# Optimization experiments

Measured on AMD Instinct MI355X. Metric: run time of the kernel, lower is better.

## Reference

```python
import jax, jax.numpy as jnp
import numpy as np

V, E, U, B, T = 128, 256, 1024, 32, 256


def setup_inputs() -> dict:
    key = jax.random.key(0)
    ks = iter(jax.random.split(key, 64))
    def p(shape, scale=0.05):
        return jax.random.normal(next(ks), shape, jnp.float32) * scale
    inp = {
        "x": jax.random.randint(next(ks), (B, T), 0, V),
        "emb": p((V, E), 1.0),
        "fc_W": p((2 * U, V)),
        "fc_b": jnp.zeros((V,), jnp.float32),
    }
    for l in range(3):
        din = E if l == 0 else 2 * U
        for d in ("fw", "bw"):
            inp[f"Wg_{d}{l}"] = p((din + U, 2 * U))   # fused r,u gate kernel
            inp[f"bg_{d}{l}"] = jnp.ones((2 * U,), jnp.float32)  # TF GRUCell ones bias init
            inp[f"Wc_{d}{l}"] = p((din + U, U))       # candidate kernel
            inp[f"bc_{d}{l}"] = jnp.zeros((U,), jnp.float32)
            inp[f"h_{d}{l}"] = jnp.zeros((B, U), jnp.float32)
    return inp


def _gru_scan(x_seq, h0, Wg, bg, Wc, bc, reverse):
    # x_seq: [T, B, din]; TF contrib GRUCell math.
    def step(h, xt):
        ru = jax.nn.sigmoid(jnp.concatenate([xt, h], -1) @ Wg + bg)
        r, u = jnp.split(ru, 2, axis=-1)
        c = jnp.tanh(jnp.concatenate([xt, r * h], -1) @ Wc + bc)
        h_new = u * h + (1.0 - u) * c
        return h_new, h_new
    hT, ys = jax.lax.scan(step, h0, x_seq, reverse=reverse)
    return hT, ys  # ys in original time order even when reverse=True


def reference(x, emb, fc_W, fc_b,
              Wg_fw0, bg_fw0, Wc_fw0, bc_fw0, h_fw0,
              Wg_bw0, bg_bw0, Wc_bw0, bc_bw0, h_bw0,
              Wg_fw1, bg_fw1, Wc_fw1, bc_fw1, h_fw1,
              Wg_bw1, bg_bw1, Wc_bw1, bc_bw1, h_bw1,
              Wg_fw2, bg_fw2, Wc_fw2, bc_fw2, h_fw2,
              Wg_bw2, bg_bw2, Wc_bw2, bc_bw2, h_bw2):
    fw = [(Wg_fw0, bg_fw0, Wc_fw0, bc_fw0, h_fw0),
          (Wg_fw1, bg_fw1, Wc_fw1, bc_fw1, h_fw1),
          (Wg_fw2, bg_fw2, Wc_fw2, bc_fw2, h_fw2)]
    bw = [(Wg_bw0, bg_bw0, Wc_bw0, bc_bw0, h_bw0),
          (Wg_bw1, bg_bw1, Wc_bw1, bc_bw1, h_bw1),
          (Wg_bw2, bg_bw2, Wc_bw2, bc_bw2, h_bw2)]
    seq = emb[x].transpose(1, 0, 2)  # [T, B, E]
    states_fw, states_bw = [], []
    for l in range(3):
        Wg, bg, Wc, bc, h0 = fw[l]
        hf, yf = _gru_scan(seq, h0, Wg, bg, Wc, bc, reverse=False)
        Wg, bg, Wc, bc, h0 = bw[l]
        hb, yb = _gru_scan(seq, h0, Wg, bg, Wc, bc, reverse=True)
        seq = jnp.concatenate([yf, yb], axis=-1)  # [T, B, 2U]
        states_fw.append(hf)
        states_bw.append(hb)
    out = seq.transpose(1, 0, 2).reshape(-1, 2 * U)  # [B*T, 2U], batch-major like dynamic_rnn
    logits = out @ fc_W + fc_b
    return (logits, jnp.stack(states_fw), jnp.stack(states_bw))
```

## Files before the change

kernel.cpp:

```cpp
#include <hip/hip_runtime.h>

typedef _Float16 f16;
typedef _Float16 f16x4 __attribute__((ext_vector_type(4)));
typedef _Float16 f16x8 __attribute__((ext_vector_type(8)));
typedef float f32x4 __attribute__((ext_vector_type(4)));

#define NB 32
#define NT 256
#define NE 256
#define NU 1024
#define NV 128

#define MEMF() asm volatile("" ::: "memory")

__device__ __forceinline__ unsigned long long cload64(const f16* p) {
    return __hip_atomic_load((const unsigned long long*)p, __ATOMIC_RELAXED,
                             __HIP_MEMORY_SCOPE_AGENT);
}
__device__ __forceinline__ float cloadf(const float* p) {
    return __hip_atomic_load(p, __ATOMIC_RELAXED, __HIP_MEMORY_SCOPE_AGENT);
}
__device__ __forceinline__ void cstoref(float* p, float v) {
    __hip_atomic_store(p, v, __ATOMIC_RELAXED, __HIP_MEMORY_SCOPE_AGENT);
}
__device__ __forceinline__ void cstore16(f16* p, f16 v) {
    __hip_atomic_store((unsigned short*)p, __builtin_bit_cast(unsigned short, v),
                       __ATOMIC_RELAXED, __HIP_MEMORY_SCOPE_AGENT);
}

__device__ __forceinline__ void barsync() {
    MEMF();
    __builtin_amdgcn_s_barrier();
    MEMF();
}

__device__ __forceinline__ void gwait(const unsigned* flagd, unsigned target) {
    if (threadIdx.x < 64) {
        int it = 0;
        for (;;) {
            unsigned v = __hip_atomic_load(&flagd[(threadIdx.x & 31) * 16],
                                           __ATOMIC_RELAXED, __HIP_MEMORY_SCOPE_AGENT);
            if (__all(v >= target)) break;
            if (++it > (1 << 16)) break;
        }
    }
}

__device__ __forceinline__ void gbar(unsigned* flagd, int cg, unsigned target) {
    asm volatile("s_waitcnt vmcnt(0)" ::: "memory");
    barsync();
    if (threadIdx.x == 0)
        __hip_atomic_store(&flagd[cg * 16], target, __ATOMIC_RELAXED,
                           __HIP_MEMORY_SCOPE_AGENT);
    gwait(flagd, target);
    barsync();
}

__device__ __forceinline__ void stage16(const f16* __restrict__ src,
                                        f16* __restrict__ stg, int tid) {
    unsigned long long a[16];
    #pragma unroll
    for (int i = 0; i < 16; ++i)
        a[i] = cload64(src + i * NU + tid * 4);
    MEMF();
    #pragma unroll
    for (int i = 0; i < 16; ++i)
        *(f16x4*)(&stg[i * 1032 + tid * 4]) = __builtin_bit_cast(f16x4, a[i]);
}

__global__ void embed_kernel(const int* __restrict__ x, const float* __restrict__ emb,
                             f16* __restrict__ seq0) {
    int row = blockIdx.x;
    int t = row >> 5, b = row & 31;
    int e = threadIdx.x;
    int idx = x[b * NT + t];
    seq0[row * NE + e] = (f16)emb[idx * NE + e];
}

__global__ void wconv(const float* __restrict__ Wg, const float* __restrict__ Wc,
                      f16* __restrict__ WgT, f16* __restrict__ WcT, int K2) {
    __shared__ float tile[32][33];
    int mat = blockIdx.z & 1;
    const float* in = mat ? Wc : Wg;
    f16* outp = mat ? WcT : WgT;
    int N = mat ? 1024 : 2048;
    int by = blockIdx.y;
    if (by * 32 >= N) return;
    int k0 = blockIdx.x * 32, n0 = by * 32;
    int tx = threadIdx.x & 31, ty = threadIdx.x >> 5;
    #pragma unroll
    for (int i = 0; i < 4; ++i) {
        int r = ty * 4 + i;
        tile[r][tx] = in[(size_t)(k0 + r) * N + n0 + tx];
    }
    __syncthreads();
    #pragma unroll
    for (int i = 0; i < 4; ++i) {
        int rn = ty * 4 + i;
        outp[(size_t)(n0 + rn) * K2 + k0 + tx] = (f16)tile[tx][rn];
    }
}

__launch_bounds__(256)
__global__ void gemm_projT(const f16* __restrict__ A, int lda, int K,
                           const f16* __restrict__ WgT, const f16* __restrict__ WcT, int K2,
                           const float* __restrict__ bg, const float* __restrict__ bc,
                           f16* __restrict__ proj) {
    __shared__ f16 As[128][40];
    __shared__ f16 Bs[128][40];
    int cb = blockIdx.y;
    const f16* Bsrc; int outcol; const float* bias;
    if (cb < 16) { Bsrc = WgT + (size_t)cb * 128 * K2; outcol = cb * 128; bias = bg + cb * 128; }
    else { Bsrc = WcT + (size_t)(cb - 16) * 128 * K2; outcol = 2048 + (cb - 16) * 128; bias = bc + (cb - 16) * 128; }
    int m0 = blockIdx.x * 128;
    int tid = threadIdx.x;
    int w = tid >> 6, l = tid & 63;
    int wm = w & 1, wn = w >> 1;
    f32x4 acc[4][4] = {};
    for (int k0 = 0; k0 < K; k0 += 32) {
        __syncthreads();
        #pragma unroll
        for (int p = 0; p < 2; ++p) {
            int e = (p * 256 + tid) * 8;
            int r = e >> 5, kq = e & 31;
            f16x8 v = *(const f16x8*)(A + (size_t)(m0 + r) * lda + k0 + kq);
            *(f16x8*)(&As[r][kq]) = v;
        }
        #pragma unroll
        for (int p = 0; p < 2; ++p) {
            int e = (p * 256 + tid) * 8;
            int r = e >> 5, kq = e & 31;
            f16x8 v = *(const f16x8*)(Bsrc + (size_t)r * K2 + k0 + kq);
            *(f16x8*)(&Bs[r][kq]) = v;
        }
        __syncthreads();
        int kq = (l >> 4) * 8;
        f16x8 a[4], b[4];
        #pragma unroll
        for (int i = 0; i < 4; ++i) a[i] = *(const f16x8*)(&As[wm * 64 + i * 16 + (l & 15)][kq]);
        #pragma unroll
        for (int j = 0; j < 4; ++j) b[j] = *(const f16x8*)(&Bs[wn * 64 + j * 16 + (l & 15)][kq]);
        #pragma unroll
        for (int i = 0; i < 4; ++i)
            #pragma unroll
            for (int j = 0; j < 4; ++j)
                acc[i][j] = __builtin_amdgcn_mfma_f32_16x16x32_f16(a[i], b[j], acc[i][j], 0, 0, 0);
    }
    int lr = (l >> 4) * 4, lc = l & 15;
    #pragma unroll
    for (int i = 0; i < 4; ++i) {
        #pragma unroll
        for (int j = 0; j < 4; ++j) {
            int gcol = wn * 64 + j * 16 + lc;
            float bia = bias[gcol];
            #pragma unroll
            for (int q = 0; q < 4; ++q) {
                int grow = m0 + wm * 64 + i * 16 + lr + q;
                proj[(size_t)grow * 3072 + outcol + gcol] = (f16)(acc[i][j][q] + bia);
            }
        }
    }
}

__launch_bounds__(256)
__global__ void gemm_proj(const f16* __restrict__ A, int lda, int K,
                          const float* __restrict__ Wg, const float* __restrict__ Wc,
                          const float* __restrict__ bg, const float* __restrict__ bc,
                          f16* __restrict__ proj) {
    __shared__ f16 As[128][40];
    __shared__ f16 Bs[128][40];
    int cb = blockIdx.y;
    const float* Bsrc; int ldb, outcol; const float* bias;
    if (cb < 16) { Bsrc = Wg + cb * 128; ldb = 2 * NU; outcol = cb * 128; bias = bg + cb * 128; }
    else { Bsrc = Wc + (cb - 16) * 128; ldb = NU; outcol = 2 * NU + (cb - 16) * 128; bias = bc + (cb - 16) * 128; }
    int m0 = blockIdx.x * 128;
    int tid = threadIdx.x;
    int w = tid >> 6, l = tid & 63;
    int wm = w & 1, wn = w >> 1;
    f32x4 acc[4][4] = {};
    for (int k0 = 0; k0 < K; k0 += 32) {
        __syncthreads();
        #pragma unroll
        for (int p = 0; p < 2; ++p) {
            int e = (p * 256 + tid) * 8;
            int r = e >> 5, kq = e & 31;
            f16x8 v = *(const f16x8*)(A + (size_t)(m0 + r) * lda + k0 + kq);
            *(f16x8*)(&As[r][kq]) = v;
        }
        #pragma unroll
        for (int p = 0; p < 4; ++p) {
            int k = p * 8 + (tid >> 5);
            int n = (tid & 31) * 4;
            float4 v = *(const float4*)(Bsrc + (size_t)(k0 + k) * ldb + n);
            Bs[n + 0][k] = (f16)v.x; Bs[n + 1][k] = (f16)v.y;
            Bs[n + 2][k] = (f16)v.z; Bs[n + 3][k] = (f16)v.w;
        }
        __syncthreads();
        int kq = (l >> 4) * 8;
        f16x8 a[4], b[4];
        #pragma unroll
        for (int i = 0; i < 4; ++i) a[i] = *(const f16x8*)(&As[wm * 64 + i * 16 + (l & 15)][kq]);
        #pragma unroll
        for (int j = 0; j < 4; ++j) b[j] = *(const f16x8*)(&Bs[wn * 64 + j * 16 + (l & 15)][kq]);
        #pragma unroll
        for (int i = 0; i < 4; ++i)
            #pragma unroll
            for (int j = 0; j < 4; ++j)
                acc[i][j] = __builtin_amdgcn_mfma_f32_16x16x32_f16(a[i], b[j], acc[i][j], 0, 0, 0);
    }
    int lr = (l >> 4) * 4, lc = l & 15;
    #pragma unroll
    for (int i = 0; i < 4; ++i) {
        #pragma unroll
        for (int j = 0; j < 4; ++j) {
            int gcol = wn * 64 + j * 16 + lc;
            float bia = bias[gcol];
            #pragma unroll
            for (int q = 0; q < 4; ++q) {
                int grow = m0 + wm * 64 + i * 16 + lr + q;
                proj[(size_t)grow * 3072 + outcol + gcol] = (f16)(acc[i][j][q] + bia);
            }
        }
    }
}

__launch_bounds__(256)
__global__ void gemm_fc(const f16* __restrict__ y, const float* __restrict__ W,
                        const float* __restrict__ bias, float* __restrict__ out) {
    __shared__ f16 As[128][40];
    __shared__ f16 Bs[128][40];
    int m0 = blockIdx.x * 128;
    int tid = threadIdx.x;
    int w = tid >> 6, l = tid & 63;
    int wm = w & 1, wn = w >> 1;
    f32x4 acc[4][4] = {};
    for (int k0 = 0; k0 < 2048; k0 += 32) {
        __syncthreads();
        #pragma unroll
        for (int p = 0; p < 2; ++p) {
            int e = (p * 256 + tid) * 8;
            int r = e >> 5, kq = e & 31;
            int grow = m0 + r;
            int b = grow >> 8, t = grow & 255;
            f16x8 v = *(const f16x8*)(y + (size_t)(t * 32 + b) * 2048 + k0 + kq);
            *(f16x8*)(&As[r][kq]) = v;
        }
        #pragma unroll
        for (int p = 0; p < 4; ++p) {
            int k = p * 8 + (tid >> 5);
            int n = (tid & 31) * 4;
            float4 v = *(const float4*)(W + (size_t)(k0 + k) * 128 + n);
            Bs[n + 0][k] = (f16)v.x; Bs[n + 1][k] = (f16)v.y;
            Bs[n + 2][k] = (f16)v.z; Bs[n + 3][k] = (f16)v.w;
        }
        __syncthreads();
        int kq = (l >> 4) * 8;
        f16x8 a[4], b[4];
        #pragma unroll
        for (int i = 0; i < 4; ++i) a[i] = *(const f16x8*)(&As[wm * 64 + i * 16 + (l & 15)][kq]);
        #pragma unroll
        for (int j = 0; j < 4; ++j) b[j] = *(const f16x8*)(&Bs[wn * 64 + j * 16 + (l & 15)][kq]);
        #pragma unroll
        for (int i = 0; i < 4; ++i)
            #pragma unroll
            for (int j = 0; j < 4; ++j)
                acc[i][j] = __builtin_amdgcn_mfma_f32_16x16x32_f16(a[i], b[j], acc[i][j], 0, 0, 0);
    }
    int lr = (l >> 4) * 4, lc = l & 15;
    #pragma unroll
    for (int i = 0; i < 4; ++i) {
        #pragma unroll
        for (int j = 0; j < 4; ++j) {
            int gcol = wn * 64 + j * 16 + lc;
            float bia = bias[gcol];
            #pragma unroll
            for (int q = 0; q < 4; ++q) {
                int grow = m0 + wm * 64 + i * 16 + lr + q;
                out[(size_t)grow * 128 + gcol] = acc[i][j][q] + bia;
            }
        }
    }
}

__launch_bounds__(256)
__global__ void gru_layer(
    const f16* __restrict__ proj_fw, const f16* __restrict__ proj_bw,
    const float* __restrict__ Wgh_fw, const float* __restrict__ Wgh_bw,
    const float* __restrict__ Wch_fw, const float* __restrict__ Wch_bw,
    const float* __restrict__ h0_fw, const float* __restrict__ h0_bw,
    f16* __restrict__ h16, f16* __restrict__ rh16, float* __restrict__ u32,
    f16* __restrict__ y, float* __restrict__ st_fw, float* __restrict__ st_bw,
    unsigned* __restrict__ cnt)
{
    extern __shared__ f16 smem[];
    f16* stg    = smem;
    f16* Wc_lds = smem + 16 * 1032;

    int bid = blockIdx.x, tid = threadIdx.x;
    int dir = bid >> 6, lb = bid & 63;
    int rh_i = lb >> 5;
    int cg   = lb & 31;
    int R0   = rh_i * 16;
    int gcb  = cg * 64;
    int ccb  = cg * 32;

    const f16*  proj = dir ? proj_bw : proj_fw;
    const float* Wgh = dir ? Wgh_bw : Wgh_fw;
    const float* Wch = dir ? Wch_bw : Wch_fw;
    const float* h0  = dir ? h0_bw  : h0_fw;
    f16*   h16d  = h16  + dir * (NB * NU);
    f16*   rh16d = rh16 + dir * (NB * NU);
    float* u32d  = u32  + dir * (NB * NU);
    unsigned* flagd = cnt + (dir * 2 + rh_i) * 1024;

    const f16* hsrc  = h16d  + (size_t)R0 * NU;
    const f16* rhsrc = rh16d + (size_t)R0 * NU;

    int w = tid >> 6, l = tid & 63;
    int lc = l & 15, lr = (l >> 4) * 4, kq = (l >> 4) * 8;

    {
        int j2 = tid & 31;
        for (int k = tid >> 5; k < NU; k += 8)
            Wc_lds[j2 * 1032 + k] = (f16)Wch[(size_t)k * 1024 + ccb + j2];
    }

    f16x8 wgf[32];
    {
        int col = gcb + w * 16 + lc;
        #pragma unroll
        for (int kt = 0; kt < 32; ++kt) {
            f16x8 t;
            #pragma unroll
            for (int e = 0; e < 8; ++e)
                t[e] = (f16)Wgh[(size_t)(kt * 32 + kq + e) * 2048 + col];
            wgf[kt] = t;
        }
    }

    {
        int base = lb * 512;
        for (int i = tid; i < 512; i += 256)
            cstore16(h16d + base + i, (f16)h0[base + i]);
    }
    f32x4 hreg = {};
    if (w < 2) {
        #pragma unroll
        for (int q = 0; q < 4; ++q)
            hreg[q] = h0[(size_t)(R0 + lr + q) * NU + ccb + w * 16 + lc];
    }

    int gc  = gcb + w * 16 + lc;
    int cc  = ccb + (w & 1) * 16 + lc;
    int cc2 = 2048 + cc;
    bool rblk = (cg < 16);

    f16 pg[4], pc[4];
    {
        int td0 = dir ? (NT - 1) : 0;
        const f16* pr = proj + (size_t)td0 * NB * 3072;
        #pragma unroll
        for (int q = 0; q < 4; ++q) {
            pg[q] = pr[(size_t)(R0 + lr + q) * 3072 + gc];
            pc[q] = pr[(size_t)(R0 + lr + q) * 3072 + cc2];
        }
    }

    unsigned bc = 1;
    gbar(flagd, cg, bc);

    for (int tl = 0; tl < NT; ++tl) {
        int td = dir ? (NT - 1 - tl) : tl;

        stage16(hsrc, stg, tid);
        asm volatile("s_waitcnt lgkmcnt(0)" ::: "memory");
        __builtin_amdgcn_sched_barrier(0);
        barsync();

        {
            const f16* ap = &stg[lc * 1032 + kq];
            f32x4 acc0 = {}, acc1 = {};
            #pragma unroll
            for (int kt = 0; kt < 32; kt += 2) {
                f16x8 a0 = *(const f16x8*)(ap + kt * 32);
                f16x8 a1 = *(const f16x8*)(ap + (kt + 1) * 32);
                acc0 = __builtin_amdgcn_mfma_f32_16x16x32_f16(a0, wgf[kt], acc0, 0, 0, 0);
                acc1 = __builtin_amdgcn_mfma_f32_16x16x32_f16(a1, wgf[kt + 1], acc1, 0, 0, 0);
            }
            f32x4 acc = acc0 + acc1;
            #pragma unroll
            for (int q = 0; q < 4; ++q) {
                int br = lr + q;
                float pre = acc[q] + (float)pg[q];
                float sg = 1.f / (1.f + __expf(-pre));
                if (rblk) {
                    float hv = (float)stg[br * 1032 + gc];
                    cstore16(rh16d + (size_t)(R0 + br) * NU + gc, (f16)(sg * hv));
                } else {
                    cstoref(u32d + (size_t)(R0 + br) * NU + gc - NU, sg);
                }
            }
        }
        ++bc;
        gbar(flagd, cg, bc);

        float uu[4];
        if (w < 2) {
            #pragma unroll
            for (int q = 0; q < 4; ++q)
                uu[q] = cloadf(u32d + (size_t)(R0 + lr + q) * NU + cc);
        }

        stage16(rhsrc, stg, tid);
        asm volatile("s_waitcnt lgkmcnt(0)" ::: "memory");
        __builtin_amdgcn_sched_barrier(0);
        barsync();

        if (w < 2) {
            const f16* ap = &stg[lc * 1032 + kq];
            const f16* bptr = Wc_lds + ((w & 1) * 16 + lc) * 1032 + kq;
            f32x4 acc0 = {}, acc1 = {};
            #pragma unroll
            for (int kt = 0; kt < 32; kt += 2) {
                f16x8 a0 = *(const f16x8*)(ap + kt * 32);
                f16x8 a1 = *(const f16x8*)(ap + (kt + 1) * 32);
                f16x8 b0 = *(const f16x8*)(bptr + kt * 32);
                f16x8 b1 = *(const f16x8*)(bptr + kt * 32 + 32);
                acc0 = __builtin_amdgcn_mfma_f32_16x16x32_f16(a0, b0, acc0, 0, 0, 0);
                acc1 = __builtin_amdgcn_mfma_f32_16x16x32_f16(a1, b1, acc1, 0, 0, 0);
            }
            f32x4 acc = acc0 + acc1;
            #pragma unroll
            for (int q = 0; q < 4; ++q) {
                int br = R0 + lr + q;
                float pre = acc[q] + (float)pc[q];
                float e2 = __expf(2.f * pre);
                float c = 1.f - 2.f / (e2 + 1.f);
                float hn = uu[q] * hreg[q] + (1.f - uu[q]) * c;
                hreg[q] = hn;
                cstore16(h16d + (size_t)br * NU + cc, (f16)hn);
            }
        }
        ++bc;
        asm volatile("s_waitcnt vmcnt(0)" ::: "memory");
        barsync();
        if (tid == 0)
            __hip_atomic_store(&flagd[cg * 16], bc, __ATOMIC_RELAXED,
                               __HIP_MEMORY_SCOPE_AGENT);
        if (w < 2) {
            #pragma unroll
            for (int q = 0; q < 4; ++q) {
                int br = R0 + lr + q;
                y[(size_t)(td * NB + br) * 2048 + dir * NU + cc] = (f16)hreg[q];
                if (tl == NT - 1)
                    (dir ? st_bw : st_fw)[(size_t)br * NU + cc] = hreg[q];
            }
        }
        if (tl + 1 < NT) {
            int tdn = dir ? (NT - 2 - tl) : (tl + 1);
            const f16* pr = proj + (size_t)tdn * NB * 3072;
            #pragma unroll
            for (int q = 0; q < 4; ++q) {
                pg[q] = pr[(size_t)(R0 + lr + q) * 3072 + gc];
                pc[q] = pr[(size_t)(R0 + lr + q) * 3072 + cc2];
            }
        }
        gwait(flagd, bc);
        barsync();
    }
}

extern "C" void kernel_launch(void* const* d_in, const int* in_sizes, int n_in,
                              void* d_out, int out_size, void* d_ws, size_t ws_size,
                              hipStream_t stream) {
    const int*   x   = (const int*)  d_in[0];
    const float* emb = (const float*)d_in[1];
    const float* fcW = (const float*)d_in[2];
    const float* fcb = (const float*)d_in[3];
    float* out = (float*)d_out;

    char* ws = (char*)d_ws;
    size_t off = 0;
    f16* seq0   = (f16*)(ws + off); off += (size_t)8192 * 256 * 2;
    f16* ybuf0  = (f16*)(ws + off); off += (size_t)8192 * 2048 * 2;
    f16* ybuf1  = (f16*)(ws + off); off += (size_t)8192 * 2048 * 2;
    f16* projfw = (f16*)(ws + off); off += (size_t)8192 * 3072 * 2;
    f16* projbw = (f16*)(ws + off); off += (size_t)8192 * 3072 * 2;
    f16*   h16  = (f16*)(ws + off);   off += 2 * 32 * 1024 * 2;
    f16*   rh16 = (f16*)(ws + off);   off += 2 * 32 * 1024 * 2;
    float* u32  = (float*)(ws + off); off += 2 * 32 * 1024 * 4;
    unsigned* ctrl = (unsigned*)(ws + off); off += 3 * 16384;
    f16* WgT_fw = (f16*)(ws + off); off += (size_t)2048 * 3072 * 2;
    f16* WgT_bw = (f16*)(ws + off); off += (size_t)2048 * 3072 * 2;
    f16* WcT_fw = (f16*)(ws + off); off += (size_t)1024 * 3072 * 2;
    f16* WcT_bw = (f16*)(ws + off); off += (size_t)1024 * 3072 * 2;
    bool cvt = (ws_size >= off);

    hipFuncSetAttribute((const void*)gru_layer,
                        hipFuncAttributeMaxDynamicSharedMemorySize, 99072);

    hipMemsetAsync(ctrl, 0, 3 * 16384, stream);
    embed_kernel<<<dim3(8192), dim3(256), 0, stream>>>(x, emb, seq0);

    const f16* lin = seq0; int lda = 256, K = 256;
    f16* ybufs[2] = {ybuf0, ybuf1};
    for (int l = 0; l < 3; ++l) {
        const float* Wg_fw = (const float*)d_in[4 + l * 10 + 0];
        const float* bg_fw = (const float*)d_in[4 + l * 10 + 1];
        const float* Wc_fw = (const float*)d_in[4 + l * 10 + 2];
        const float* bc_fw = (const float*)d_in[4 + l * 10 + 3];
        const float* h0_fw = (const float*)d_in[4 + l * 10 + 4];
        const float* Wg_bw = (const float*)d_in[4 + l * 10 + 5];
        const float* bg_bw = (const float*)d_in[4 + l * 10 + 6];
        const float* Wc_bw = (const float*)d_in[4 + l * 10 + 7];
        const float* bc_bw = (const float*)d_in[4 + l * 10 + 8];
        const float* h0_bw = (const float*)d_in[4 + l * 10 + 9];
        int din = (l == 0) ? 256 : 2048;
        int K2 = din + 1024;

        if (cvt) {
            wconv<<<dim3(K2 / 32, 64, 2), dim3(256), 0, stream>>>(Wg_fw, Wc_fw, WgT_fw, WcT_fw, K2);
            wconv<<<dim3(K2 / 32, 64, 2), dim3(256), 0, stream>>>(Wg_bw, Wc_bw, WgT_bw, WcT_bw, K2);
            gemm_projT<<<dim3(64, 24), dim3(256), 0, stream>>>(lin, lda, K, WgT_fw, WcT_fw, K2, bg_fw, bc_fw, projfw);
            gemm_projT<<<dim3(64, 24), dim3(256), 0, stream>>>(lin, lda, K, WgT_bw, WcT_bw, K2, bg_bw, bc_bw, projbw);
        } else {
            gemm_proj<<<dim3(64, 24), dim3(256), 0, stream>>>(lin, lda, K, Wg_fw, Wc_fw, bg_fw, bc_fw, projfw);
            gemm_proj<<<dim3(64, 24), dim3(256), 0, stream>>>(lin, lda, K, Wg_bw, Wc_bw, bg_bw, bc_bw, projbw);
        }

        const float* Wgh_fw = Wg_fw + (size_t)din * 2048;
        const float* Wgh_bw = Wg_bw + (size_t)din * 2048;
        const float* Wch_fw = Wc_fw + (size_t)din * 1024;
        const float* Wch_bw = Wc_bw + (size_t)din * 1024;
        f16* yout = ybufs[l & 1];
        float* stfw = out + 1048576 + l * 32768;
        float* stbw = out + 1048576 + 98304 + l * 32768;
        unsigned* cnt = ctrl + l * 4096;

        gru_layer<<<dim3(128), dim3(256), 99072, stream>>>(
            projfw, projbw, Wgh_fw, Wgh_bw, Wch_fw, Wch_bw, h0_fw, h0_bw,
            h16, rh16, u32, yout, stfw, stbw, cnt);
        lin = yout; lda = 2048; K = 2048;
    }

    gemm_fc<<<dim3(64), dim3(256), 0, stream>>>(ybufs[0], fcW, fcb, out);
}
```

Measured before the change: 5.765 ms.

## Pin GRU cooperative groups to single XCDs and use L2-local sync when verified

Launches 256 blocks and has each block read its XCC ID and register itself, so each 32-block cooperative group (one direction and one row half) lives on a single XCD. Surplus blocks exit. A runtime handshake checks that plain stores and sc0 loads are visible within the group. If the check passes, the recurrent loop switches to non-atomic stores and sc0-only loads for flags, h, r*h and u, so the traffic stays in the shared per-XCD L2 rather than going through device-coherent paths. The aim is to cut the latency of the two grid barriers per timestep. The cost is a more fragile dependence on hardware block placement, a fallback path, and a lower spin-timeout limit.

```diff
diff --git a/kernel.cpp b/kernel.cpp
--- a/kernel.cpp
+++ b/kernel.cpp
@@ -13,6 +13,8 @@
 
 #define MEMF() asm volatile("" ::: "memory")
 
+template<bool B> struct BoolT { static constexpr bool value = B; };
+
 __device__ __forceinline__ unsigned long long cload64(const f16* p) {
     return __hip_atomic_load((const unsigned long long*)p, __ATOMIC_RELAXED,
                              __HIP_MEMORY_SCOPE_AGENT);
@@ -34,30 +36,29 @@
     MEMF();
 }
 
-__device__ __forceinline__ void gwait(const unsigned* flagd, unsigned target) {
-    if (threadIdx.x < 64) {
-        int it = 0;
-        for (;;) {
-            unsigned v = __hip_atomic_load(&flagd[(threadIdx.x & 31) * 16],
-                                           __ATOMIC_RELAXED, __HIP_MEMORY_SCOPE_AGENT);
-            if (__all(v >= target)) break;
-            if (++it > (1 << 16)) break;
-        }
-    }
-}
-
-__device__ __forceinline__ void gbar(unsigned* flagd, int cg, unsigned target) {
-    asm volatile("s_waitcnt vmcnt(0)" ::: "memory");
-    barsync();
-    if (threadIdx.x == 0)
-        __hip_atomic_store(&flagd[cg * 16], target, __ATOMIC_RELAXED,
-                           __HIP_MEMORY_SCOPE_AGENT);
-    gwait(flagd, target);
-    barsync();
-}
-
-__device__ __forceinline__ void stage16(const f16* __restrict__ src,
-                                        f16* __restrict__ stg, int tid) {
+__device__ __forceinline__ unsigned ld_sc0_wait(const unsigned* p) {
+    unsigned v;
+    asm volatile("global_load_dword %0, %1, off sc0\n\ts_waitcnt vmcnt(0)"
+                 : "=&v"(v) : "v"(p) : "memory");
+    return v;
+}
+__device__ __forceinline__ void ld4f_sc0(const float* p0, const float* p1,
+                                         const float* p2, const float* p3, float* o) {
+    asm volatile(
+        "global_load_dword %0, %4, off sc0\n\t"
+        "global_load_dword %1, %5, off sc0\n\t"
+        "global_load_dword %2, %6, off sc0\n\t"
+        "global_load_dword %3, %7, off sc0\n\t"
+        "s_waitcnt vmcnt(0)"
+        : "=&v"(o[0]), "=&v"(o[1]), "=&v"(o[2]), "=&v"(o[3])
+        : "v"(p0), "v"(p1), "v"(p2), "v"(p3) : "memory");
+}
+__device__ __forceinline__ void st_plain_u32(unsigned* p, unsigned t) {
+    asm volatile("global_store_dword %0, %1, off" :: "v"(p), "v"(t) : "memory");
+}
+
+__device__ __forceinline__ void stage16s(const f16* __restrict__ src,
+                                         f16* __restrict__ stg, int tid) {
     unsigned long long a[16];
     #pragma unroll
     for (int i = 0; i < 16; ++i)
@@ -66,6 +67,72 @@
     #pragma unroll
     for (int i = 0; i < 16; ++i)
         *(f16x4*)(&stg[i * 1032 + tid * 4]) = __builtin_bit_cast(f16x4, a[i]);
+}
+__device__ __forceinline__ void stage16f(const f16* __restrict__ src,
+                                         f16* __restrict__ stg, int tid) {
+    const char* b = (const char*)(src + tid * 4);
+    unsigned long long o0,o1,o2,o3,o4,o5,o6,o7,o8,o9,o10,o11,o12,o13,o14,o15;
+    asm volatile(
+        "global_load_dwordx2 %[v0],  %[a0], off sc0\n\t"
+        "global_load_dwordx2 %[v1],  %[a0], off offset:2048 sc0\n\t"
+        "global_load_dwordx2 %[v2],  %[a1], off sc0\n\t"
+        "global_load_dwordx2 %[v3],  %[a1], off offset:2048 sc0\n\t"
+        "global_load_dwordx2 %[v4],  %[a2], off sc0\n\t"
+        "global_load_dwordx2 %[v5],  %[a2], off offset:2048 sc0\n\t"
+        "global_load_dwordx2 %[v6],  %[a3], off sc0\n\t"
+        "global_load_dwordx2 %[v7],  %[a3], off offset:2048 sc0\n\t"
+        "global_load_dwordx2 %[v8],  %[a4], off sc0\n\t"
+        "global_load_dwordx2 %[v9],  %[a4], off offset:2048 sc0\n\t"
+        "global_load_dwordx2 %[v10], %[a5], off sc0\n\t"
+        "global_load_dwordx2 %[v11], %[a5], off offset:2048 sc0\n\t"
+        "global_load_dwordx2 %[v12], %[a6], off sc0\n\t"
+        "global_load_dwordx2 %[v13], %[a6], off offset:2048 sc0\n\t"
+        "global_load_dwordx2 %[v14], %[a7], off sc0\n\t"
+        "global_load_dwordx2 %[v15], %[a7], off offset:2048 sc0\n\t"
+        "s_waitcnt vmcnt(0)"
+        : [v0]"=&v"(o0), [v1]"=&v"(o1), [v2]"=&v"(o2), [v3]"=&v"(o3),
+          [v4]"=&v"(o4), [v5]"=&v"(o5), [v6]"=&v"(o6), [v7]"=&v"(o7),
+          [v8]"=&v"(o8), [v9]"=&v"(o9), [v10]"=&v"(o10), [v11]"=&v"(o11),
+          [v12]"=&v"(o12), [v13]"=&v"(o13), [v14]"=&v"(o14), [v15]"=&v"(o15)
+        : [a0]"v"(b), [a1]"v"(b + 4096), [a2]"v"(b + 8192), [a3]"v"(b + 12288),
+          [a4]"v"(b + 16384), [a5]"v"(b + 20480), [a6]"v"(b + 24576), [a7]"v"(b + 28672)
+        : "memory");
+    unsigned long long oo[16] = {o0,o1,o2,o3,o4,o5,o6,o7,o8,o9,o10,o11,o12,o13,o14,o15};
+    #pragma unroll
+    for (int i = 0; i < 16; ++i)
+        *(f16x4*)(&stg[i * 1032 + tid * 4]) = __builtin_bit_cast(f16x4, oo[i]);
+}
+
+template<bool F> __device__ __forceinline__ void gwaitx(const unsigned* fF,
+                                                        const unsigned* fS, unsigned t) {
+    if (threadIdx.x < 64) {
+        int lane = threadIdx.x & 31;
+        int it = 0;
+        for (;;) {
+            unsigned v;
+            if constexpr (F) v = ld_sc0_wait(fF + lane * 16);
+            else             v = __hip_atomic_load(fS + lane * 16, __ATOMIC_RELAXED,
+                                                   __HIP_MEMORY_SCOPE_AGENT);
+            if (__all(v >= t)) break;
+            if (++it > 8192) break;
+        }
+    }
+}
+template<bool F> __device__ __forceinline__ void arrivex(unsigned* fF, unsigned* fS,
+                                                         int cg, unsigned t) {
+    if (threadIdx.x == 0) {
+        if constexpr (F) st_plain_u32(fF + cg * 16, t);
+        else __hip_atomic_store(fS + cg * 16, t, __ATOMIC_RELAXED,
+                                __HIP_MEMORY_SCOPE_AGENT);
+    }
+}
+template<bool F> __device__ __forceinline__ void gbarx(unsigned* fF, unsigned* fS,
+                                                       int cg, unsigned t) {
+    asm volatile("s_waitcnt vmcnt(0)" ::: "memory");
+    barsync();
+    arrivex<F>(fF, fS, cg, t);
+    gwaitx<F>(fF, fS, t);
+    barsync();
 }
 
 __global__ void embed_kernel(const int* __restrict__ x, const float* __restrict__ emb,
@@ -290,19 +357,42 @@
     const float* __restrict__ h0_fw, const float* __restrict__ h0_bw,
     f16* __restrict__ h16, f16* __restrict__ rh16, float* __restrict__ u32,
     f16* __restrict__ y, float* __restrict__ st_fw, float* __restrict__ st_bw,
-    unsigned* __restrict__ cnt)
+    unsigned* __restrict__ ctrl)
 {
     extern __shared__ f16 smem[];
     f16* stg    = smem;
     f16* Wc_lds = smem + 16 * 1032;
-
-    int bid = blockIdx.x, tid = threadIdx.x;
-    int dir = bid >> 6, lb = bid & 63;
-    int rh_i = lb >> 5;
-    int cg   = lb & 31;
-    int R0   = rh_i * 16;
-    int gcb  = cg * 64;
-    int ccb  = cg * 32;
+    __shared__ int s_c, s_cg, s_ok;
+
+    int tid = threadIdx.x;
+    unsigned* regc = ctrl;
+
+    if (tid == 0) {
+        unsigned xcc;
+        asm volatile("s_getreg_b32 %0, hwreg(HW_REG_XCC_ID)" : "=s"(xcc));
+        xcc &= 7u;
+        unsigned rk = __hip_atomic_fetch_add(&regc[xcc * 16], 1u,
+                                             __ATOMIC_RELAXED, __HIP_MEMORY_SCOPE_AGENT);
+        int c = -1;
+        if (xcc < 4u && rk < 32u) {
+            int it = 0;
+            while (__hip_atomic_load(&regc[xcc * 16], __ATOMIC_RELAXED,
+                                     __HIP_MEMORY_SCOPE_AGENT) < 32u) {
+                if (++it > (1 << 14)) break;
+            }
+            c = (int)xcc;
+        }
+        s_c = c; s_cg = (int)rk;
+    }
+    barsync();
+    int c = s_c;
+    if (c < 0) return;
+    int cg = s_cg;
+
+    int dir = c >> 1, rh_i = c & 1;
+    int R0  = rh_i * 16;
+    int gcb = cg * 64;
+    int ccb = cg * 32;
 
     const f16*  proj = dir ? proj_bw : proj_fw;
     const float* Wgh = dir ? Wgh_bw : Wgh_fw;
@@ -311,7 +401,11 @@
     f16*   h16d  = h16  + dir * (NB * NU);
     f16*   rh16d = rh16 + dir * (NB * NU);
     float* u32d  = u32  + dir * (NB * NU);
-    unsigned* flagd = cnt + (dir * 2 + rh_i) * 1024;
+    unsigned* cbase = ctrl + 128 + c * 2048;
+    unsigned* fF    = cbase;
+    unsigned* fS    = cbase + 512;
+    unsigned* chk   = cbase + 1024;
+    unsigned* vote  = cbase + 1536;
 
     const f16* hsrc  = h16d  + (size_t)R0 * NU;
     const f16* rhsrc = rh16d + (size_t)R0 * NU;
@@ -339,9 +433,9 @@
     }
 
     {
-        int base = lb * 512;
+        int base2 = (rh_i * 32 + cg) * 512;
         for (int i = tid; i < 512; i += 256)
-            cstore16(h16d + base + i, (f16)h0[base + i]);
+            cstore16(h16d + base2 + i, (f16)h0[base2 + i]);
     }
     f32x4 hreg = {};
     if (w < 2) {
@@ -366,108 +460,152 @@
         }
     }
 
-    unsigned bc = 1;
-    gbar(flagd, cg, bc);
-
-    for (int tl = 0; tl < NT; ++tl) {
-        int td = dir ? (NT - 1 - tl) : tl;
-
-        stage16(hsrc, stg, tid);
-        asm volatile("s_waitcnt lgkmcnt(0)" ::: "memory");
-        __builtin_amdgcn_sched_barrier(0);
-        barsync();
-
-        {
-            const f16* ap = &stg[lc * 1032 + kq];
-            f32x4 acc0 = {}, acc1 = {};
-            #pragma unroll
-            for (int kt = 0; kt < 32; kt += 2) {
-                f16x8 a0 = *(const f16x8*)(ap + kt * 32);
-                f16x8 a1 = *(const f16x8*)(ap + (kt + 1) * 32);
-                acc0 = __builtin_amdgcn_mfma_f32_16x16x32_f16(a0, wgf[kt], acc0, 0, 0, 0);
-                acc1 = __builtin_amdgcn_mfma_f32_16x16x32_f16(a1, wgf[kt + 1], acc1, 0, 0, 0);
-            }
-            f32x4 acc = acc0 + acc1;
-            #pragma unroll
-            for (int q = 0; q < 4; ++q) {
-                int br = lr + q;
-                float pre = acc[q] + (float)pg[q];
-                float sg = 1.f / (1.f + __expf(-pre));
-                if (rblk) {
-                    float hv = (float)stg[br * 1032 + gc];
-                    cstore16(rh16d + (size_t)(R0 + br) * NU + gc, (f16)(sg * hv));
-                } else {
-                    cstoref(u32d + (size_t)(R0 + br) * NU + gc - NU, sg);
+    unsigned bc = 0;
+    if (tid == 0)
+        st_plain_u32(chk + cg * 16, 0xA5000000u | ((unsigned)c << 8) | (unsigned)cg);
+    ++bc; gbarx<false>(fF, fS, cg, bc);
+    int okA = 1, okB = 1;
+    if (tid < 64) {
+        unsigned v = ld_sc0_wait(chk + (tid & 31) * 16);
+        okA = __all(v == (0xA5000000u | ((unsigned)c << 8) | (unsigned)(tid & 31)));
+    }
+    if (tid == 0)
+        st_plain_u32(chk + cg * 16, 0x5A000000u | ((unsigned)c << 8) | (unsigned)cg);
+    ++bc; gbarx<false>(fF, fS, cg, bc);
+    if (tid < 64) {
+        unsigned v = ld_sc0_wait(chk + (tid & 31) * 16);
+        okB = __all(v == (0x5A000000u | ((unsigned)c << 8) | (unsigned)(tid & 31)));
+    }
+    if (tid == 0)
+        __hip_atomic_store(vote + cg * 16, (okA && okB) ? 2u : 1u,
+                           __ATOMIC_RELAXED, __HIP_MEMORY_SCOPE_AGENT);
+    ++bc; gbarx<false>(fF, fS, cg, bc);
+    if (tid < 64) {
+        unsigned v = __hip_atomic_load(vote + (tid & 31) * 16, __ATOMIC_RELAXED,
+                                       __HIP_MEMORY_SCOPE_AGENT);
+        int ok = __all(v == 2u);
+        if (tid == 0) s_ok = ok;
+    }
+    barsync();
+    int fastmode = s_ok;
+
+    auto run = [&](auto tag) {
+        constexpr bool F = decltype(tag)::value;
+        for (int tl = 0; tl < NT; ++tl) {
+            int td = dir ? (NT - 1 - tl) : tl;
+
+            if constexpr (F) stage16f(hsrc, stg, tid);
+            else             stage16s(hsrc, stg, tid);
+            asm volatile("s_waitcnt lgkmcnt(0)" ::: "memory");
+            __builtin_amdgcn_sched_barrier(0);
+            barsync();
+
+            {
+                const f16* ap = &stg[lc * 1032 + kq];
+                f32x4 acc0 = {}, acc1 = {};
+                #pragma unroll
+                for (int kt = 0; kt < 32; kt += 2) {
+                    f16x8 a0 = *(const f16x8*)(ap + kt * 32);
+                    f16x8 a1 = *(const f16x8*)(ap + (kt + 1) * 32);
+                    acc0 = __builtin_amdgcn_mfma_f32_16x16x32_f16(a0, wgf[kt], acc0, 0, 0, 0);
+                    acc1 = __builtin_amdgcn_mfma_f32_16x16x32_f16(a1, wgf[kt + 1], acc1, 0, 0, 0);
                 }
-            }
-        }
-        ++bc;
-        gbar(flagd, cg, bc);
-
-        float uu[4];
-        if (w < 2) {
-            #pragma unroll
-            for (int q = 0; q < 4; ++q)
-                uu[q] = cloadf(u32d + (size_t)(R0 + lr + q) * NU + cc);
-        }
-
-        stage16(rhsrc, stg, tid);
-        asm volatile("s_waitcnt lgkmcnt(0)" ::: "memory");
-        __builtin_amdgcn_sched_barrier(0);
-        barsync();
-
-        if (w < 2) {
-            const f16* ap = &stg[lc * 1032 + kq];
-            const f16* bptr = Wc_lds + ((w & 1) * 16 + lc) * 1032 + kq;
-            f32x4 acc0 = {}, acc1 = {};
-            #pragma unroll
-            for (int kt = 0; kt < 32; kt += 2) {
-                f16x8 a0 = *(const f16x8*)(ap + kt * 32);
-                f16x8 a1 = *(const f16x8*)(ap + (kt + 1) * 32);
-                f16x8 b0 = *(const f16x8*)(bptr + kt * 32);
-                f16x8 b1 = *(const f16x8*)(bptr + kt * 32 + 32);
-                acc0 = __builtin_amdgcn_mfma_f32_16x16x32_f16(a0, b0, acc0, 0, 0, 0);
-                acc1 = __builtin_amdgcn_mfma_f32_16x16x32_f16(a1, b1, acc1, 0, 0, 0);
-            }
-            f32x4 acc = acc0 + acc1;
-            #pragma unroll
-            for (int q = 0; q < 4; ++q) {
-                int br = R0 + lr + q;
-                float pre = acc[q] + (float)pc[q];
-                float e2 = __expf(2.f * pre);
-                float c = 1.f - 2.f / (e2 + 1.f);
-                float hn = uu[q] * hreg[q] + (1.f - uu[q]) * c;
-                hreg[q] = hn;
-                cstore16(h16d + (size_t)br * NU + cc, (f16)hn);
-            }
-        }
-        ++bc;
-        asm volatile("s_waitcnt vmcnt(0)" ::: "memory");
-        barsync();
-        if (tid == 0)
-            __hip_atomic_store(&flagd[cg * 16], bc, __ATOMIC_RELAXED,
-                               __HIP_MEMORY_SCOPE_AGENT);
-        if (w < 2) {
-            #pragma unroll
-            for (int q = 0; q < 4; ++q) {
-                int br = R0 + lr + q;
-                y[(size_t)(td * NB + br) * 2048 + dir * NU + cc] = (f16)hreg[q];
-                if (tl == NT - 1)
-                    (dir ? st_bw : st_fw)[(size_t)br * NU + cc] = hreg[q];
-            }
-        }
-        if (tl + 1 < NT) {
-            int tdn = dir ? (NT - 2 - tl) : (tl + 1);
-            const f16* pr = proj + (size_t)tdn * NB * 3072;
-            #pragma unroll
-            for (int q = 0; q < 4; ++q) {
-                pg[q] = pr[(size_t)(R0 + lr + q) * 3072 + gc];
-                pc[q] = pr[(size_t)(R0 + lr + q) * 3072 + cc2];
-            }
-        }
-        gwait(flagd, bc);
-        barsync();
-    }
+                f32x4 acc = acc0 + acc1;
+                #pragma unroll
+                for (int q = 0; q < 4; ++q) {
+                    int br = lr + q;
+                    float pre = acc[q] + (float)pg[q];
+                    float sg = 1.f / (1.f + __expf(-pre));
+                    if (rblk) {
+                        float hv = (float)stg[br * 1032 + gc];
+                        f16 v = (f16)(sg * hv);
+                        if constexpr (F) rh16d[(size_t)(R0 + br) * NU + gc] = v;
+                        else             cstore16(rh16d + (size_t)(R0 + br) * NU + gc, v);
+                    } else {
+                        if constexpr (F) u32d[(size_t)(R0 + br) * NU + gc - NU] = sg;
+                        else             cstoref(u32d + (size_t)(R0 + br) * NU + gc - NU, sg);
+                    }
+                }
+            }
+            ++bc;
+            gbarx<F>(fF, fS, cg, bc);
+
+            float uu[4];
+            if constexpr (F) {
+                const float* p0 = (w < 2) ? u32d + (size_t)(R0 + lr + 0) * NU + cc : u32d;
+                const float* p1 = (w < 2) ? u32d + (size_t)(R0 + lr + 1) * NU + cc : u32d;
+                const float* p2 = (w < 2) ? u32d + (size_t)(R0 + lr + 2) * NU + cc : u32d;
+                const float* p3 = (w < 2) ? u32d + (size_t)(R0 + lr + 3) * NU + cc : u32d;
+                ld4f_sc0(p0, p1, p2, p3, uu);
+            } else {
+                if (w < 2) {
+                    #pragma unroll
+                    for (int q = 0; q < 4; ++q)
+                        uu[q] = cloadf(u32d + (size_t)(R0 + lr + q) * NU + cc);
+                }
+            }
+
+            if constexpr (F) stage16f(rhsrc, stg, tid);
+            else             stage16s(rhsrc, stg, tid);
+            asm volatile("s_waitcnt lgkmcnt(0)" ::: "memory");
+            __builtin_amdgcn_sched_barrier(0);
+            barsync();
+
+            if (w < 2) {
+                const f16* ap = &stg[lc * 1032 + kq];
+                const f16* bptr = Wc_lds + ((w & 1) * 16 + lc) * 1032 + kq;
+                f32x4 acc0 = {}, acc1 = {};
+                #pragma unroll
+                for (int kt = 0; kt < 32; kt += 2) {
+                    f16x8 a0 = *(const f16x8*)(ap + kt * 32);
+                    f16x8 a1 = *(const f16x8*)(ap + (kt + 1) * 32);
+                    f16x8 b0 = *(const f16x8*)(bptr + kt * 32);
+                    f16x8 b1 = *(const f16x8*)(bptr + kt * 32 + 32);
+                    acc0 = __builtin_amdgcn_mfma_f32_16x16x32_f16(a0, b0, acc0, 0, 0, 0);
+                    acc1 = __builtin_amdgcn_mfma_f32_16x16x32_f16(a1, b1, acc1, 0, 0, 0);
+                }
+                f32x4 acc = acc0 + acc1;
+                #pragma unroll
+                for (int q = 0; q < 4; ++q) {
+                    int br = R0 + lr + q;
+                    float pre = acc[q] + (float)pc[q];
+                    float e2 = __expf(2.f * pre);
+                    float cv = 1.f - 2.f / (e2 + 1.f);
+                    float hn = uu[q] * hreg[q] + (1.f - uu[q]) * cv;
+                    hreg[q] = hn;
+                    f16 hv = (f16)hn;
+                    if constexpr (F) h16d[(size_t)br * NU + cc] = hv;
+                    else             cstore16(h16d + (size_t)br * NU + cc, hv);
+                }
+            }
+            ++bc;
+            asm volatile("s_waitcnt vmcnt(0)" ::: "memory");
+            barsync();
+            arrivex<F>(fF, fS, cg, bc);
+            if (w < 2) {
+                #pragma unroll
+                for (int q = 0; q < 4; ++q) {
+                    int br = R0 + lr + q;
+                    y[(size_t)(td * NB + br) * 2048 + dir * NU + cc] = (f16)hreg[q];
+                    if (tl == NT - 1)
+                        (dir ? st_bw : st_fw)[(size_t)br * NU + cc] = hreg[q];
+                }
+            }
+            if (tl + 1 < NT) {
+                int tdn = dir ? (NT - 2 - tl) : (tl + 1);
+                const f16* pr = proj + (size_t)tdn * NB * 3072;
+                #pragma unroll
+                for (int q = 0; q < 4; ++q) {
+                    pg[q] = pr[(size_t)(R0 + lr + q) * 3072 + gc];
+                    pc[q] = pr[(size_t)(R0 + lr + q) * 3072 + cc2];
+                }
+            }
+            gwaitx<F>(fF, fS, bc);
+            barsync();
+        }
+    };
+    if (fastmode) run(BoolT<true>{});
+    else          run(BoolT<false>{});
 }
 
 extern "C" void kernel_launch(void* const* d_in, const int* in_sizes, int n_in,
@@ -489,7 +627,7 @@
     f16*   h16  = (f16*)(ws + off);   off += 2 * 32 * 1024 * 2;
     f16*   rh16 = (f16*)(ws + off);   off += 2 * 32 * 1024 * 2;
     float* u32  = (float*)(ws + off); off += 2 * 32 * 1024 * 4;
-    unsigned* ctrl = (unsigned*)(ws + off); off += 3 * 16384;
+    unsigned* ctrl = (unsigned*)(ws + off); off += 3 * 49152;
     f16* WgT_fw = (f16*)(ws + off); off += (size_t)2048 * 3072 * 2;
     f16* WgT_bw = (f16*)(ws + off); off += (size_t)2048 * 3072 * 2;
     f16* WcT_fw = (f16*)(ws + off); off += (size_t)1024 * 3072 * 2;
@@ -499,7 +637,7 @@
     hipFuncSetAttribute((const void*)gru_layer,
                         hipFuncAttributeMaxDynamicSharedMemorySize, 99072);
 
-    hipMemsetAsync(ctrl, 0, 3 * 16384, stream);
+    hipMemsetAsync(ctrl, 0, 3 * 49152, stream);
     embed_kernel<<<dim3(8192), dim3(256), 0, stream>>>(x, emb, seq0);
 
     const f16* lin = seq0; int lda = 256, K = 256;
@@ -535,9 +673,9 @@
         f16* yout = ybufs[l & 1];
         float* stfw = out + 1048576 + l * 32768;
         float* stbw = out + 1048576 + 98304 + l * 32768;
-        unsigned* cnt = ctrl + l * 4096;
-
-        gru_layer<<<dim3(128), dim3(256), 99072, stream>>>(
+        unsigned* cnt = ctrl + l * 12288;
+
+        gru_layer<<<dim3(256), dim3(256), 99072, stream>>>(
             projfw, projbw, Wgh_fw, Wgh_bw, Wch_fw, Wch_bw, h0_fw, h0_bw,
             h16, rh16, u32, yout, stfw, stbw, cnt);
         lin = yout; lda = 2048; K = 2048;
```

After: 11.53 ms. 2x slower.
